# Kernel tuning notes

Hardware: AMD Instinct MI355X
Metric: run time of the kernel (lower is better)

Reference implementation:

```python
import jax, jax.numpy as jnp
import numpy as np

B, P, ENC, DEC, ATT, E, V, L = 32, 196, 2048, 512, 512, 256, 30000, 21


def setup_inputs() -> dict:
    key = jax.random.key(0)
    ks = jax.random.split(key, 24)
    n = lambda k, shape, s=0.02: (jax.random.normal(k, shape, jnp.float32) * s)
    return {
        "encoder_out": jax.random.normal(ks[0], (B, P, ENC), jnp.float32),
        "captions": jax.random.randint(ks[1], (B, L), 0, V, jnp.int64),
        "caption_lengths": jax.random.randint(ks[2], (B,), 1, L, jnp.int64),
        "emb": n(ks[3], (V, E)),
        "We_att": n(ks[4], (ATT, ENC)), "be_att": jnp.zeros((ATT,), jnp.float32),
        "Wd_att": n(ks[5], (ATT, DEC)), "bd_att": jnp.zeros((ATT,), jnp.float32),
        "Wf_att": n(ks[6], (1, ATT)),  "bf_att": jnp.zeros((1,), jnp.float32),
        "W_ih": n(ks[7], (4 * DEC, E + ENC)), "b_ih": jnp.zeros((4 * DEC,), jnp.float32),
        "W_hh": n(ks[8], (4 * DEC, DEC)),     "b_hh": jnp.zeros((4 * DEC,), jnp.float32),
        "W_fc": n(ks[9], (V, DEC)), "b_fc": jnp.zeros((V,), jnp.float32),
        "W_h0": n(ks[10], (DEC, ENC)), "b_h0": jnp.zeros((DEC,), jnp.float32),
        "W_c0": n(ks[11], (DEC, ENC)), "b_c0": jnp.zeros((DEC,), jnp.float32),
    }


def reference(encoder_out, captions, caption_lengths, emb, We_att, be_att,
              Wd_att, bd_att, Wf_att, bf_att, W_ih, b_ih, W_hh, b_hh,
              W_fc, b_fc, W_h0, b_h0, W_c0, b_c0):
    # init hidden state from mean-pooled encoder features
    mean_enc = encoder_out.mean(axis=1)                      # [B, ENC]
    h = mean_enc @ W_h0.T + b_h0                             # [B, DEC]
    c = mean_enc @ W_c0.T + b_c0                             # [B, DEC]

    # encoder projection for attention is step-invariant: compute once
    att1 = jnp.einsum("bpe,ae->bpa", encoder_out, We_att) + be_att  # [B,P,ATT]

    embs = emb[captions]                                     # [B, L, E]
    decode_len = captions.shape[1] - 1
    xs = jnp.swapaxes(embs[:, :decode_len, :], 0, 1)         # [T, B, E]

    def step(carry, emb_t):
        h, c = carry
        # Bahdanau attention
        att2 = h @ Wd_att.T + bd_att                         # [B, ATT]
        combined = jnp.maximum(att1 + att2[:, None, :], 0.0) # [B, P, ATT]
        e = jnp.einsum("bpa,a->bp", combined, Wf_att[0]) + bf_att[0]
        alpha = jax.nn.softmax(e, axis=1)                    # [B, P]
        awe = jnp.einsum("bpe,bp->be", encoder_out, alpha)   # [B, ENC]
        # single-layer LSTM cell (PyTorch gate order: i, f, g, o)
        x = jnp.concatenate([emb_t, awe], axis=1)            # [B, E+ENC]
        gates = x @ W_ih.T + b_ih + h @ W_hh.T + b_hh        # [B, 4*DEC]
        i, f, g, o = jnp.split(gates, 4, axis=1)
        c_new = jax.nn.sigmoid(f) * c + jax.nn.sigmoid(i) * jnp.tanh(g)
        h_new = jax.nn.sigmoid(o) * jnp.tanh(c_new)
        # dropout in eval mode = identity
        preds = h_new @ W_fc.T + b_fc                        # [B, V]
        return (h_new, c_new), (preds, alpha)

    (_, _), (preds_t, alphas_t) = jax.lax.scan(step, (h, c), xs)
    predictions = jnp.swapaxes(preds_t, 0, 1)                # [B, T, V]
    alphas = jnp.swapaxes(alphas_t, 0, 1)                    # [B, T, P]
    return predictions, alphas
```

## Files before the change

kernel.cpp:

```cpp
#include <hip/hip_runtime.h>

#define B    32
#define P    196
#define ENC  2048
#define DEC  512
#define ATT  512
#define E    256
#define V    30000
#define VPAD 30080
#define L    21
#define T    20
#define KX   2304

typedef unsigned short u16;
typedef __bf16 bf16x8 __attribute__((ext_vector_type(8)));
typedef float  f32x4  __attribute__((ext_vector_type(4)));

__device__ __forceinline__ u16 f2bf(float f) {
    union { float f; unsigned int i; } v; v.f = f;
    unsigned int i = v.i;
    return (u16)((i + 0x7fffu + ((i >> 16) & 1u)) >> 16);
}
__device__ __forceinline__ float bf2f(u16 u) {
    union { unsigned int i; float f; } v; v.i = ((unsigned int)u) << 16; return v.f;
}
__device__ __forceinline__ float wave_sum(float v) {
    #pragma unroll
    for (int o = 32; o > 0; o >>= 1) v += __shfl_down(v, o, 64);
    return v;
}
__device__ __forceinline__ float sigf(float x) { return 1.0f / (1.0f + expf(-x)); }

__device__ __forceinline__ int xcd_swizzle(int bid, int nwg) {
    int xcd = bid & 7, idx = bid >> 3;
    int q = nwg >> 3, r = nwg & 7;
    return (xcd < r ? xcd * (q + 1) : r * (q + 1) + (xcd - r) * q) + idx;
}

__device__ __forceinline__ void gl2lds16(const u16* g, char* l) {
    __builtin_amdgcn_global_load_lds(
        (const __attribute__((address_space(1))) void*)g,
        (__attribute__((address_space(3))) void*)l, 16, 0, 0);
}

__global__ void k_f2b4(const float* __restrict__ s, u16* __restrict__ d, int n4) {
    int i = blockIdx.x * 256 + threadIdx.x;
    if (i < n4) {
        float4 v = reinterpret_cast<const float4*>(s)[i];
        ushort4 o;
        o.x = f2bf(v.x); o.y = f2bf(v.y); o.z = f2bf(v.z); o.w = f2bf(v.w);
        reinterpret_cast<ushort4*>(d)[i] = o;
    }
}

__global__ void k_zero16(u16* __restrict__ d, int n) {
    int i = blockIdx.x * 256 + threadIdx.x;
    if (i < n) d[i] = 0;
}

__global__ void k_mean(const float* __restrict__ enc, float* __restrict__ mean) {
    int idx = blockIdx.x * 256 + threadIdx.x;
    int b = idx >> 11, e = idx & 2047;
    const float* p = enc + (size_t)b * P * ENC + e;
    float s = 0.f;
    for (int i = 0; i < P; i++) s += p[(size_t)i * ENC];
    mean[idx] = s * (1.0f / 196.0f);
}

__global__ void k_h0c0(const float* __restrict__ mean,
                       const float* __restrict__ Wh0, const float* __restrict__ bh0,
                       const float* __restrict__ Wc0, const float* __restrict__ bc0,
                       u16* __restrict__ h, float* __restrict__ c) {
    int wid = (blockIdx.x * 256 + threadIdx.x) >> 6;
    int lane = threadIdx.x & 63;
    int b = wid >> 10, j = wid & 1023;
    bool is_h = j < DEC;
    int jj = is_h ? j : j - DEC;
    const float* W = is_h ? Wh0 : Wc0;
    const float* mrow = mean + b * ENC;
    const float* wrow = W + (size_t)jj * ENC;
    float acc = 0.f;
    #pragma unroll
    for (int kk = 0; kk < 4; kk++) {
        int k = kk * 512 + lane * 8;
        float4 a0 = *reinterpret_cast<const float4*>(mrow + k);
        float4 a1 = *reinterpret_cast<const float4*>(mrow + k + 4);
        float4 w0 = *reinterpret_cast<const float4*>(wrow + k);
        float4 w1 = *reinterpret_cast<const float4*>(wrow + k + 4);
        acc += a0.x * w0.x + a0.y * w0.y + a0.z * w0.z + a0.w * w0.w;
        acc += a1.x * w1.x + a1.y * w1.y + a1.z * w1.z + a1.w * w1.w;
    }
    acc = wave_sum(acc);
    if (lane == 0) {
        acc += is_h ? bh0[jj] : bc0[jj];
        if (is_h) h[b * DEC + jj] = f2bf(acc);
        else      c[b * DEC + jj] = acc;
    }
}

template<int K, bool PREDS>
__global__ __launch_bounds__(256) void k_gemm128(
        const u16* __restrict__ A, const u16* __restrict__ Bmat,
        const float* __restrict__ bias, float* __restrict__ Cout) {
    __shared__ char smem[32768];
    char* As = smem;
    char* Bs = smem + 16384;
    int g = xcd_swizzle(blockIdx.x, gridDim.x);
    int bm, bn;
    if constexpr (PREDS) { bm = g % 5; bn = g / 5; }
    else                 { bm = g >> 2; bn = g & 3; }
    int tid  = threadIdx.x;
    int w    = tid >> 6, lane = tid & 63;
    int quad = lane >> 4, l16 = lane & 15;
    int wave_m = (w >> 1) * 64, wave_n = (w & 1) * 64;

    int rl = lane >> 3;
    int ce = (((lane & 7) << 4) ^ (rl << 4)) >> 1;
    const u16* srcA[4]; const u16* srcB[4];
    char* dstA[4]; char* dstB[4];
    #pragma unroll
    for (int i = 0; i < 4; i++) {
        int r = i * 32 + w * 8 + rl;
        srcA[i] = A    + (size_t)(bm * 128 + r) * K + ce;
        srcB[i] = Bmat + (size_t)(bn * 128 + r) * K + ce;
        dstA[i] = As + i * 4096 + w * 1024;
        dstB[i] = Bs + i * 4096 + w * 1024;
    }

    f32x4 acc[4][4] = {};
    int swz = (l16 & 7) << 4;
    for (int kt = 0; kt < K / 64; kt++) {
        int koff = kt * 64;
        #pragma unroll
        for (int i = 0; i < 4; i++) {
            gl2lds16(srcA[i] + koff, dstA[i]);
            gl2lds16(srcB[i] + koff, dstB[i]);
        }
        __syncthreads();
        #pragma unroll
        for (int ks = 0; ks < 2; ks++) {
            int cb = ks * 64 + quad * 16;
            bf16x8 av[4], bv[4];
            #pragma unroll
            for (int mi = 0; mi < 4; mi++) {
                int r = wave_m + mi * 16 + l16;
                av[mi] = *reinterpret_cast<const bf16x8*>(As + r * 128 + (cb ^ swz));
            }
            #pragma unroll
            for (int ni = 0; ni < 4; ni++) {
                int r = wave_n + ni * 16 + l16;
                bv[ni] = *reinterpret_cast<const bf16x8*>(Bs + r * 128 + (cb ^ swz));
            }
            #pragma unroll
            for (int mi = 0; mi < 4; mi++)
                #pragma unroll
                for (int ni = 0; ni < 4; ni++)
                    acc[mi][ni] = __builtin_amdgcn_mfma_f32_16x16x32_bf16(
                        av[mi], bv[ni], acc[mi][ni], 0, 0, 0);
        }
        __syncthreads();
    }

    #pragma unroll
    for (int mi = 0; mi < 4; mi++) {
        #pragma unroll
        for (int ni = 0; ni < 4; ni++) {
            int nn = bn * 128 + wave_n + ni * 16 + l16;
            float bv = (!PREDS || nn < V) ? bias[nn] : 0.f;
            #pragma unroll
            for (int r = 0; r < 4; r++) {
                int mm = bm * 128 + wave_m + mi * 16 + quad * 4 + r;
                if constexpr (PREDS) {
                    if (nn < V) {
                        int b = mm & 31, t = mm >> 5;
                        Cout[(size_t)b * T * V + (size_t)t * V + nn] = acc[mi][ni][r] + bv;
                    }
                } else {
                    Cout[(size_t)mm * ATT + nn] = acc[mi][ni][r] + bv;
                }
            }
        }
    }
}

__global__ void k_att2(const u16* __restrict__ h, const float* __restrict__ Wd,
                       const float* __restrict__ bd, float* __restrict__ att2) {
    int wid = (blockIdx.x * 256 + threadIdx.x) >> 6;
    int lane = threadIdx.x & 63;
    int b = wid >> 9, a = wid & 511;
    bf16x8 hv = *reinterpret_cast<const bf16x8*>(h + b * DEC + lane * 8);
    const float4* wd = reinterpret_cast<const float4*>(Wd + (size_t)a * DEC + lane * 8);
    float4 w0 = wd[0], w1 = wd[1];
    float acc = (float)hv[0] * w0.x + (float)hv[1] * w0.y + (float)hv[2] * w0.z + (float)hv[3] * w0.w
              + (float)hv[4] * w1.x + (float)hv[5] * w1.y + (float)hv[6] * w1.z + (float)hv[7] * w1.w;
    acc = wave_sum(acc);
    if (lane == 0) att2[b * ATT + a] = acc + bd[a];
}

__global__ void k_e(const float* __restrict__ att1, const float* __restrict__ att2,
                    const float* __restrict__ Wf, const float* __restrict__ bf,
                    float* __restrict__ e) {
    int wid = (blockIdx.x * 256 + threadIdx.x) >> 6;
    int lane = threadIdx.x & 63;
    int b = wid / P, p = wid % P;
    const float* a1 = att1 + ((size_t)b * P + p) * ATT + lane * 8;
    const float* a2 = att2 + b * ATT + lane * 8;
    const float* wf = Wf + lane * 8;
    float acc = 0.f;
    #pragma unroll
    for (int j = 0; j < 8; j++) {
        float v = a1[j] + a2[j];
        v = v > 0.f ? v : 0.f;
        acc += v * wf[j];
    }
    acc = wave_sum(acc);
    if (lane == 0) e[b * P + p] = acc + bf[0];
}

__global__ __launch_bounds__(256) void k_smawe(
        const float* __restrict__ ew, const u16* __restrict__ enc_bf,
        const float* __restrict__ emb, const int* __restrict__ caps,
        u16* __restrict__ xbuf, float* __restrict__ out_alpha, int t) {
    __shared__ float sm[256];
    __shared__ float al[256];
    int bid = blockIdx.x, tid = threadIdx.x;
    int b = bid >> 3, chunk = bid & 7;
    float v = (tid < P) ? ew[b * P + tid] : -1e30f;
    sm[tid] = v; __syncthreads();
    for (int s = 128; s > 0; s >>= 1) {
        if (tid < s) sm[tid] = fmaxf(sm[tid], sm[tid + s]);
        __syncthreads();
    }
    float mx = sm[0]; __syncthreads();
    float evv = (tid < P) ? expf(v - mx) : 0.f;
    sm[tid] = evv; __syncthreads();
    for (int s = 128; s > 0; s >>= 1) {
        if (tid < s) sm[tid] += sm[tid + s];
        __syncthreads();
    }
    float inv = 1.0f / sm[0];
    float aa = evv * inv;
    al[tid] = aa;
    if (chunk == 0 && tid < P)
        out_alpha[(size_t)b * T * P + (size_t)t * P + tid] = aa;
    __syncthreads();
    int ec = (chunk << 8) + tid;
    const u16* ep = enc_bf + (size_t)b * P * ENC + ec;
    float acc = 0.f;
    #pragma unroll 4
    for (int p = 0; p < P; p++) acc += al[p] * bf2f(ep[(size_t)p * ENC]);
    xbuf[b * KX + E + ec] = f2bf(acc);
    if (chunk == 0) {
        int cap = caps[b * L + t];
        xbuf[b * KX + tid] = f2bf(emb[(size_t)cap * E + tid]);
    }
}

__global__ __launch_bounds__(256) void k_gatesK(
        const u16* __restrict__ xbuf, const u16* __restrict__ h,
        const u16* __restrict__ Wih, const u16* __restrict__ Whh,
        float* __restrict__ gpart) {
    int bid = blockIdx.x;
    int kq = bid >> 6, mt = (bid >> 5) & 1, jt = bid & 31;
    int tid = threadIdx.x, wg = tid >> 6, lane = tid & 63;
    int quad = lane >> 4, l16 = lane & 15;
    int m = mt * 16 + l16;
    int n = (wg << 9) + (jt << 4) + l16;
    f32x4 acc = {0.f, 0.f, 0.f, 0.f};
    int k0 = kq * 704;
    for (int ks = 0; ks < 22; ks++) {
        int kb = k0 + ks * 32;
        bf16x8 av, bv;
        if (kb < KX) {
            av = *reinterpret_cast<const bf16x8*>(xbuf + m * KX + kb + (quad << 3));
            bv = *reinterpret_cast<const bf16x8*>(Wih + (size_t)n * KX + kb + (quad << 3));
        } else {
            av = *reinterpret_cast<const bf16x8*>(h + m * DEC + (kb - KX) + (quad << 3));
            bv = *reinterpret_cast<const bf16x8*>(Whh + (size_t)n * DEC + (kb - KX) + (quad << 3));
        }
        acc = __builtin_amdgcn_mfma_f32_16x16x32_bf16(av, bv, acc, 0, 0, 0);
    }
    #pragma unroll
    for (int r = 0; r < 4; r++) {
        int gm = mt * 16 + (quad << 2) + r;
        gpart[((kq << 5) + gm) * 2048 + n] = acc[r];
    }
}

__global__ void k_cell(const float* __restrict__ gpart,
                       const float* __restrict__ bih, const float* __restrict__ bhh,
                       float* __restrict__ cbuf, u16* __restrict__ hn,
                       u16* __restrict__ hall, int t) {
    int gtid = blockIdx.x * 256 + threadIdx.x;
    int d = gtid & 511;
    int b = gtid >> 9;
    float g0 = bih[d]        + bhh[d];
    float g1 = bih[512 + d]  + bhh[512 + d];
    float g2 = bih[1024 + d] + bhh[1024 + d];
    float g3 = bih[1536 + d] + bhh[1536 + d];
    #pragma unroll
    for (int kq = 0; kq < 4; kq++) {
        const float* gp = gpart + ((kq << 5) + b) * 2048;
        g0 += gp[d]; g1 += gp[512 + d]; g2 += gp[1024 + d]; g3 += gp[1536 + d];
    }
    float gi = sigf(g0), gf = sigf(g1), gg = tanhf(g2), go = sigf(g3);
    float cn = gf * cbuf[gtid] + gi * gg;
    cbuf[gtid] = cn;
    u16 hbv = f2bf(go * tanhf(cn));
    hn[gtid] = hbv;
    hall[(size_t)t * B * DEC + gtid] = hbv;
}

extern "C" void kernel_launch(void* const* d_in, const int* in_sizes, int n_in,
                              void* d_out, int out_size, void* d_ws, size_t ws_size,
                              hipStream_t stream) {
    const float* enc  = (const float*)d_in[0];
    const int*   caps = (const int*)d_in[1];
    const float* emb  = (const float*)d_in[3];
    const float* We   = (const float*)d_in[4];
    const float* be   = (const float*)d_in[5];
    const float* Wd   = (const float*)d_in[6];
    const float* bd   = (const float*)d_in[7];
    const float* Wf   = (const float*)d_in[8];
    const float* bfa  = (const float*)d_in[9];
    const float* Wih  = (const float*)d_in[10];
    const float* bih  = (const float*)d_in[11];
    const float* Whh  = (const float*)d_in[12];
    const float* bhh  = (const float*)d_in[13];
    const float* Wfc  = (const float*)d_in[14];
    const float* bfc  = (const float*)d_in[15];
    const float* Wh0  = (const float*)d_in[16];
    const float* bh0  = (const float*)d_in[17];
    const float* Wc0  = (const float*)d_in[18];
    const float* bc0  = (const float*)d_in[19];

    float* out_preds = (float*)d_out;
    float* out_alpha = (float*)d_out + (size_t)B * T * V;

    char* w = (char*)d_ws;
    size_t off = 0;
    auto carve = [&](size_t bytes) -> void* {
        void* p = w + off;
        off = (off + bytes + 255) & ~(size_t)255;
        return p;
    };
    u16*   enc_bf = (u16*)  carve((size_t)B * P * ENC * 2);
    u16*   We_bf  = (u16*)  carve((size_t)ATT * ENC * 2);
    u16*   Wih_bf = (u16*)  carve((size_t)4 * DEC * KX * 2);
    u16*   Whh_bf = (u16*)  carve((size_t)4 * DEC * DEC * 2);
    u16*   Wfc_bf = (u16*)  carve((size_t)VPAD * DEC * 2);
    float* att1   = (float*)carve((size_t)B * P * ATT * 4);
    float* meanb  = (float*)carve((size_t)B * ENC * 4);
    float* att2w  = (float*)carve((size_t)B * ATT * 4);
    float* ebuf   = (float*)carve((size_t)B * P * 4);
    u16*   xbuf   = (u16*)  carve((size_t)B * KX * 2);
    u16*   hb0    = (u16*)  carve((size_t)B * DEC * 2);
    u16*   hb1    = (u16*)  carve((size_t)B * DEC * 2);
    float* cbuf   = (float*)carve((size_t)B * DEC * 4);
    u16*   hall   = (u16*)  carve((size_t)T * B * DEC * 2);
    float* gpart  = (float*)carve((size_t)4 * B * 4 * DEC * 4);
    (void)ws_size; (void)n_in; (void)in_sizes; (void)out_size;

    k_f2b4<<<(B * P * ENC) / 1024, 256, 0, stream>>>(enc, enc_bf, (B * P * ENC) / 4);
    k_f2b4<<<(ATT * ENC) / 1024, 256, 0, stream>>>(We, We_bf, (ATT * ENC) / 4);
    k_f2b4<<<(4 * DEC * KX) / 1024, 256, 0, stream>>>(Wih, Wih_bf, (4 * DEC * KX) / 4);
    k_f2b4<<<(4 * DEC * DEC) / 1024, 256, 0, stream>>>(Whh, Whh_bf, (4 * DEC * DEC) / 4);
    k_f2b4<<<(V * DEC) / 1024, 256, 0, stream>>>(Wfc, Wfc_bf, (V * DEC) / 4);
    k_zero16<<<((VPAD - V) * DEC) / 256, 256, 0, stream>>>(Wfc_bf + (size_t)V * DEC, (VPAD - V) * DEC);

    k_mean<<<(B * ENC) / 256, 256, 0, stream>>>(enc, meanb);
    k_h0c0<<<(B * 2 * DEC * 64) / 256, 256, 0, stream>>>(meanb, Wh0, bh0, Wc0, bc0, hb0, cbuf);
    k_gemm128<ENC, false><<<(B * P / 128) * (ATT / 128), 256, 0, stream>>>(enc_bf, We_bf, be, att1);

    for (int t = 0; t < T; t++) {
        const u16* hin = (t & 1) ? hb1 : hb0;
        u16* hnx = (t & 1) ? hb0 : hb1;
        k_att2  <<<(B * ATT * 64) / 256, 256, 0, stream>>>(hin, Wd, bd, att2w);
        k_e     <<<(B * P * 64) / 256, 256, 0, stream>>>(att1, att2w, Wf, bfa, ebuf);
        k_smawe <<<B * 8, 256, 0, stream>>>(ebuf, enc_bf, emb, caps, xbuf, out_alpha, t);
        k_gatesK<<<256, 256, 0, stream>>>(xbuf, hin, Wih_bf, Whh_bf, gpart);
        k_cell  <<<64, 256, 0, stream>>>(gpart, bih, bhh, cbuf, hnx, hall, t);
    }

    k_gemm128<DEC, true><<<5 * (VPAD / 128), 256, 0, stream>>>(hall, Wfc_bf, bfc, out_preds);
}
```

Baseline: 1.155 ms.

## Fuse LSTM cell, att2 projection and attention scores into one per-step kernel

Replaces the per-step k_att2, k_e and k_cell launches with a fused kernel k_A, leaving three launches per timestep instead of five. In k_A, each block of 8 per batch row redundantly finishes the previous step's LSTM cell from gate partials. It then computes a 64-column slice of the decoder attention projection in shared memory and writes partial attention scores over that ATT slice. k_B sums those partial scores before the softmax. The cell state is double-buffered so the redundant blocks can work concurrently, and a final k_cell after the loop produces the last hidden state. The aim is to cut launch overhead and intermediate global traffic on the serial recurrence, at the cost of duplicating the cell math across blocks.

```diff
diff --git a/kernel.cpp b/kernel.cpp
--- a/kernel.cpp
+++ b/kernel.cpp
@@ -11,6 +11,7 @@
 #define L    21
 #define T    20
 #define KX   2304
+#define EPS  224
 
 typedef unsigned short u16;
 typedef __bf16 bf16x8 __attribute__((ext_vector_type(8)));
@@ -183,49 +184,92 @@
     }
 }
 
-__global__ void k_att2(const u16* __restrict__ h, const float* __restrict__ Wd,
-                       const float* __restrict__ bd, float* __restrict__ att2) {
-    int wid = (blockIdx.x * 256 + threadIdx.x) >> 6;
-    int lane = threadIdx.x & 63;
-    int b = wid >> 9, a = wid & 511;
-    bf16x8 hv = *reinterpret_cast<const bf16x8*>(h + b * DEC + lane * 8);
-    const float4* wd = reinterpret_cast<const float4*>(Wd + (size_t)a * DEC + lane * 8);
-    float4 w0 = wd[0], w1 = wd[1];
-    float acc = (float)hv[0] * w0.x + (float)hv[1] * w0.y + (float)hv[2] * w0.z + (float)hv[3] * w0.w
-              + (float)hv[4] * w1.x + (float)hv[5] * w1.y + (float)hv[6] * w1.z + (float)hv[7] * w1.w;
-    acc = wave_sum(acc);
-    if (lane == 0) att2[b * ATT + a] = acc + bd[a];
-}
-
-__global__ void k_e(const float* __restrict__ att1, const float* __restrict__ att2,
-                    const float* __restrict__ Wf, const float* __restrict__ bf,
-                    float* __restrict__ e) {
-    int wid = (blockIdx.x * 256 + threadIdx.x) >> 6;
-    int lane = threadIdx.x & 63;
-    int b = wid / P, p = wid % P;
-    const float* a1 = att1 + ((size_t)b * P + p) * ATT + lane * 8;
-    const float* a2 = att2 + b * ATT + lane * 8;
-    const float* wf = Wf + lane * 8;
-    float acc = 0.f;
-    #pragma unroll
-    for (int j = 0; j < 8; j++) {
-        float v = a1[j] + a2[j];
-        v = v > 0.f ? v : 0.f;
-        acc += v * wf[j];
-    }
-    acc = wave_sum(acc);
-    if (lane == 0) e[b * P + p] = acc + bf[0];
-}
-
-__global__ __launch_bounds__(256) void k_smawe(
-        const float* __restrict__ ew, const u16* __restrict__ enc_bf,
-        const float* __restrict__ emb, const int* __restrict__ caps,
-        u16* __restrict__ xbuf, float* __restrict__ out_alpha, int t) {
+__global__ __launch_bounds__(256) void k_A(
+        const float* __restrict__ att1, const float* __restrict__ Wd,
+        const float* __restrict__ bd,   const float* __restrict__ Wf,
+        const u16* __restrict__ h0,     const float* __restrict__ gpart,
+        const float* __restrict__ bih,  const float* __restrict__ bhh,
+        const float* __restrict__ c_in, float* __restrict__ c_out,
+        u16* __restrict__ hout, u16* __restrict__ hall,
+        float* __restrict__ epart, int t) {
+    __shared__ u16  hs[DEC];
+    __shared__ float att2s[64];
+    int bid = blockIdx.x;
+    int b = bid >> 3, ac = bid & 7;
+    int tid = threadIdx.x;
+    int w = tid >> 6, lane = tid & 63;
+
+    if (t == 0) {
+        hs[tid]       = h0[b * DEC + tid];
+        hs[tid + 256] = h0[b * DEC + tid + 256];
+    } else {
+        #pragma unroll
+        for (int i = 0; i < 2; i++) {
+            int d = tid + i * 256;
+            float g0 = bih[d]        + bhh[d];
+            float g1 = bih[512 + d]  + bhh[512 + d];
+            float g2 = bih[1024 + d] + bhh[1024 + d];
+            float g3 = bih[1536 + d] + bhh[1536 + d];
+            #pragma unroll
+            for (int kq = 0; kq < 4; kq++) {
+                const float* gp = gpart + ((kq << 5) + b) * 2048;
+                g0 += gp[d]; g1 += gp[512 + d]; g2 += gp[1024 + d]; g3 += gp[1536 + d];
+            }
+            float gi = sigf(g0), gf = sigf(g1), gg = tanhf(g2), go = sigf(g3);
+            int idx = b * DEC + d;
+            float cn = gf * c_in[idx] + gi * gg;
+            c_out[idx] = cn;
+            u16 hv = f2bf(go * tanhf(cn));
+            hs[d] = hv;
+            hout[idx] = hv;
+            hall[(size_t)(t - 1) * B * DEC + idx] = hv;
+        }
+    }
+    __syncthreads();
+
+    float hf[8];
+    #pragma unroll
+    for (int j = 0; j < 8; j++) hf[j] = bf2f(hs[lane * 8 + j]);
+    #pragma unroll 4
+    for (int i = 0; i < 16; i++) {
+        int al = w * 16 + i;
+        int a  = ac * 64 + al;
+        const float* wd = Wd + (size_t)a * DEC + lane * 8;
+        float4 w0 = *reinterpret_cast<const float4*>(wd);
+        float4 w1 = *reinterpret_cast<const float4*>(wd + 4);
+        float acc = hf[0]*w0.x + hf[1]*w0.y + hf[2]*w0.z + hf[3]*w0.w
+                  + hf[4]*w1.x + hf[5]*w1.y + hf[6]*w1.z + hf[7]*w1.w;
+        acc = wave_sum(acc);
+        if (lane == 0) att2s[al] = acc + bd[a];
+    }
+    __syncthreads();
+
+    float wfv = Wf[ac * 64 + lane];
+    float a2v = att2s[lane];
+    for (int p = w; p < P; p += 4) {
+        float x = att1[((size_t)b * P + p) * ATT + ac * 64 + lane];
+        float v = fmaxf(x + a2v, 0.f) * wfv;
+        v = wave_sum(v);
+        if (lane == 0) epart[bid * EPS + p] = v;
+    }
+}
+
+__global__ __launch_bounds__(256) void k_B(
+        const float* __restrict__ epart, const u16* __restrict__ enc_bf,
+        const float* __restrict__ emb,   const int* __restrict__ caps,
+        const float* __restrict__ bfa,   u16* __restrict__ xbuf,
+        float* __restrict__ out_alpha, int t) {
     __shared__ float sm[256];
     __shared__ float al[256];
     int bid = blockIdx.x, tid = threadIdx.x;
     int b = bid >> 3, chunk = bid & 7;
-    float v = (tid < P) ? ew[b * P + tid] : -1e30f;
+    float v;
+    if (tid < P) {
+        float s = bfa[0];
+        #pragma unroll
+        for (int c = 0; c < 8; c++) s += epart[(b * 8 + c) * EPS + tid];
+        v = s;
+    } else v = -1e30f;
     sm[tid] = v; __syncthreads();
     for (int s = 128; s > 0; s >>= 1) {
         if (tid < s) sm[tid] = fmaxf(sm[tid], sm[tid + s]);
@@ -351,12 +395,12 @@
     u16*   Wfc_bf = (u16*)  carve((size_t)VPAD * DEC * 2);
     float* att1   = (float*)carve((size_t)B * P * ATT * 4);
     float* meanb  = (float*)carve((size_t)B * ENC * 4);
-    float* att2w  = (float*)carve((size_t)B * ATT * 4);
-    float* ebuf   = (float*)carve((size_t)B * P * 4);
+    float* epart  = (float*)carve((size_t)256 * EPS * 4);
     u16*   xbuf   = (u16*)  carve((size_t)B * KX * 2);
     u16*   hb0    = (u16*)  carve((size_t)B * DEC * 2);
     u16*   hb1    = (u16*)  carve((size_t)B * DEC * 2);
-    float* cbuf   = (float*)carve((size_t)B * DEC * 4);
+    float* cb0    = (float*)carve((size_t)B * DEC * 4);
+    float* cb1    = (float*)carve((size_t)B * DEC * 4);
     u16*   hall   = (u16*)  carve((size_t)T * B * DEC * 2);
     float* gpart  = (float*)carve((size_t)4 * B * 4 * DEC * 4);
     (void)ws_size; (void)n_in; (void)in_sizes; (void)out_size;
@@ -369,18 +413,19 @@
     k_zero16<<<((VPAD - V) * DEC) / 256, 256, 0, stream>>>(Wfc_bf + (size_t)V * DEC, (VPAD - V) * DEC);
 
     k_mean<<<(B * ENC) / 256, 256, 0, stream>>>(enc, meanb);
-    k_h0c0<<<(B * 2 * DEC * 64) / 256, 256, 0, stream>>>(meanb, Wh0, bh0, Wc0, bc0, hb0, cbuf);
+    k_h0c0<<<(B * 2 * DEC * 64) / 256, 256, 0, stream>>>(meanb, Wh0, bh0, Wc0, bc0, hb0, cb0);
     k_gemm128<ENC, false><<<(B * P / 128) * (ATT / 128), 256, 0, stream>>>(enc_bf, We_bf, be, att1);
 
     for (int t = 0; t < T; t++) {
-        const u16* hin = (t & 1) ? hb1 : hb0;
-        u16* hnx = (t & 1) ? hb0 : hb1;
-        k_att2  <<<(B * ATT * 64) / 256, 256, 0, stream>>>(hin, Wd, bd, att2w);
-        k_e     <<<(B * P * 64) / 256, 256, 0, stream>>>(att1, att2w, Wf, bfa, ebuf);
-        k_smawe <<<B * 8, 256, 0, stream>>>(ebuf, enc_bf, emb, caps, xbuf, out_alpha, t);
-        k_gatesK<<<256, 256, 0, stream>>>(xbuf, hin, Wih_bf, Whh_bf, gpart);
-        k_cell  <<<64, 256, 0, stream>>>(gpart, bih, bhh, cbuf, hnx, hall, t);
-    }
+        u16*   hcur  = (t & 1) ? hb1 : hb0;
+        const float* c_in  = (t & 1) ? cb0 : cb1;
+        float*       c_out = (t & 1) ? cb1 : cb0;
+        k_A    <<<256, 256, 0, stream>>>(att1, Wd, bd, Wf, hb0, gpart, bih, bhh,
+                                         c_in, c_out, hcur, hall, epart, t);
+        k_B    <<<256, 256, 0, stream>>>(epart, enc_bf, emb, caps, bfa, xbuf, out_alpha, t);
+        k_gatesK<<<256, 256, 0, stream>>>(xbuf, hcur, Wih_bf, Whh_bf, gpart);
+    }
+    k_cell<<<64, 256, 0, stream>>>(gpart, bih, bhh, cb1, hb0, hall, T - 1);
 
     k_gemm128<DEC, true><<<5 * (VPAD / 128), 256, 0, stream>>>(hall, Wfc_bf, bfc, out_preds);
 }
```

New measurement: 1.625 ms. +40.6%, slower.
